# Optimization experiments

Measured on AMD Instinct MI355X. Metric: run time of the kernel, lower is better.

The kernel has to match this reference:

```python
import jax, jax.numpy as jnp
import numpy as np

# Config constants (MLAConfig)
B, S = 1, 2048                 # batch, context_len (prefill: seq == context_len)
H = 16                         # num_heads
DN, DR, DV = 128, 64, 128      # qk_nope_head_dim, qk_rope_head_dim, v_head_dim
QL, C = 1536, 512              # q_lora_rank, kv_lora_rank
BLK = 128                      # fp8 dequant block size
MAX_CACHE = 4096
SOFTMAX_SCALE = 1.0 / np.sqrt(DN + DR)  # 1/sqrt(192)
NEG_INF = -10000.0


def gen_rope(n_total, head_size):
    # theta_j = 10000^{-2j/d}; idx_theta[i, 0, :] = [i*theta, i*theta] (repeated halves)
    theta = 1.0 / (10000.0 ** (jnp.arange(0, head_size, 2, dtype=jnp.float32) / head_size))
    idx = jnp.outer(jnp.arange(n_total, dtype=jnp.float32), theta)  # (N, d/2)
    return jnp.tile(idx[:, None, :], (1, 1, 2))                     # (N, 1, d)


def fp8_dequant(x, s, block=BLK):
    # Block-wise dequant: x (M,N) * per-(block x block) scale s (M/b, N/b).
    M, N = x.shape
    m, n = M // block, N // block  # shapes chosen divisible by block -> no padding
    return (x.reshape(m, block, n, block) * s[:, None, :, None]).reshape(M, N)


def apply_rope(x, cos, sin):
    # x: (B*S, heads, d). Interleaved RoPE: de-interleave pairs into halves,
    # then x*cos + rotate_half(x)*sin with cos/sin (B*S, 1, d).
    bs, h, d = x.shape
    x = x.reshape(bs, h, d // 2, 2).transpose(0, 1, 3, 2).reshape(bs, h, d)
    rot = jnp.concatenate([-x[..., d // 2:], x[..., :d // 2]], axis=-1)
    return x * cos + rot * sin


def setup_inputs() -> dict:
    key = jax.random.key(0)
    ks = jax.random.split(key, 9)
    WUQ = jax.random.normal(ks[0], (H * (DN + DR), QL), dtype=jnp.float32)
    WUKV = jax.random.normal(ks[1], (H * (DN + DV), C), dtype=jnp.float32)
    # positive, small block scales so attention logits stay well-conditioned
    WUQ_scale = 0.05 * jax.random.uniform(ks[2], (H * (DN + DR) // BLK, QL // BLK), dtype=jnp.float32)
    WUKV_scale = 0.05 * jax.random.uniform(ks[3], (H * (DN + DV) // BLK, C // BLK), dtype=jnp.float32)
    Q = jax.random.normal(ks[4], (B, S, QL), dtype=jnp.float32)
    KV = jax.random.normal(ks[5], (B, S, C), dtype=jnp.float32)
    PE = jax.random.normal(ks[6], (B, S, DR), dtype=jnp.float32)
    kv_cache = jax.random.normal(ks[7], (B, MAX_CACHE, C), dtype=jnp.float32)
    pe_cache = jax.random.normal(ks[8], (B, MAX_CACHE, DR), dtype=jnp.float32)
    idx_theta = gen_rope(B * S, DR)
    mask = jnp.triu(jnp.full((S, S), NEG_INF, dtype=jnp.float32), k=1)
    return {"WUQ": WUQ, "WUQ_scale": WUQ_scale, "WUKV": WUKV, "WUKV_scale": WUKV_scale,
            "Q": Q, "KV": KV, "PE": PE, "kv_cache": kv_cache, "pe_cache": pe_cache,
            "idx_theta": idx_theta, "mask": mask}


def reference(WUQ, WUQ_scale, WUKV, WUKV_scale, Q, KV, PE, kv_cache, pe_cache, idx_theta, mask):
    bsz, seqlen, _ = Q.shape
    # fp8 block-wise dequant of the low-rank up-projection weights
    WUQd = fp8_dequant(WUQ, WUQ_scale)
    WUKVd = fp8_dequant(WUKV, WUKV_scale)
    # Q up-projection from q_lora latent: (B*S, QL) @ (QL, H*(DN+DR))
    q = (Q.reshape(-1, QL) @ WUQd.T).reshape(bsz, seqlen, H, DN + DR)
    q_nope, q_pe = q[..., :DN], q[..., DN:]
    cos, sin = jnp.cos(idx_theta), jnp.sin(idx_theta)  # (B*S, 1, DR)
    q_pe = apply_rope(q_pe.reshape(bsz * seqlen, H, DR), cos, sin).reshape(bsz, seqlen, H, DR)
    k_pe = apply_rope(PE.reshape(bsz * seqlen, 1, DR), cos, sin).reshape(bsz, seqlen, DR)
    # absorbed low-rank K matrix: q_nope projected into the kv latent space
    W3 = WUKVd.reshape(H, DN + DV, C)
    q_lat = jnp.einsum('bshd,hdc->bshc', q_nope, W3[:, :DN])
    # continuous-cache prefill: write fresh latents into the cache, attend over them
    kv = kv_cache.at[:, :seqlen].set(KV)[:, :seqlen]   # (B, S, C)
    pe = pe_cache.at[:, :seqlen].set(k_pe)[:, :seqlen]  # (B, S, DR)
    scores = (jnp.einsum('bshc,btc->bsht', q_lat, kv)
              + jnp.einsum('bshr,btr->bsht', q_pe, pe)) * SOFTMAX_SCALE
    scores = scores + mask[None, :, None, :]
    attn = jax.nn.softmax(scores, axis=-1)
    x = jnp.einsum('bsht,btc->bshc', attn, kv)
    out = jnp.einsum('bshc,hdc->bshd', x, W3[:, DN:])  # V up-projection (absorbed)
    return out  # (B, S, H, DV)
```

## Files before the change

### kernel.cpp

```cpp
#include <hip/hip_runtime.h>

typedef __bf16 bf16_t;
typedef __attribute__((ext_vector_type(4))) __bf16 bf16x4;
typedef __attribute__((ext_vector_type(8))) __bf16 bf16x8;
typedef __attribute__((ext_vector_type(4))) float f32x4;

#define SOFTMAX_SCALE 0.07216878364870322f
#define NEG_MASK (-10000.0f)

__device__ __forceinline__ void async16(const bf16_t* g, bf16_t* l) {
  __builtin_amdgcn_global_load_lds(
      (const __attribute__((address_space(1))) unsigned int*)g,
      (__attribute__((address_space(3))) unsigned int*)l, 16, 0, 0);
}


__global__ void k_dequant(const float* __restrict__ W, const float* __restrict__ S,
                          bf16_t* __restrict__ out, int cols, int scols) {
  int i = (blockIdx.x * 256 + threadIdx.x) * 4;
  int r = i / cols, c = i % cols;
  float s = S[(r >> 7) * scols + (c >> 7)];
  float4 w = *(const float4*)(W + i);
  out[i + 0] = (bf16_t)(w.x * s);
  out[i + 1] = (bf16_t)(w.y * s);
  out[i + 2] = (bf16_t)(w.z * s);
  out[i + 3] = (bf16_t)(w.w * s);
}

__global__ void k_f32_to_bf16(const float* __restrict__ in, bf16_t* __restrict__ out) {
  int i = (blockIdx.x * 256 + threadIdx.x) * 4;
  float4 v = *(const float4*)(in + i);
  out[i + 0] = (bf16_t)(v.x * SOFTMAX_SCALE);
  out[i + 1] = (bf16_t)(v.y * SOFTMAX_SCALE);
  out[i + 2] = (bf16_t)(v.z * SOFTMAX_SCALE);
  out[i + 3] = (bf16_t)(v.w * SOFTMAX_SCALE);
}

__global__ void k_wv1t(const bf16_t* __restrict__ Wd, bf16_t* __restrict__ Wt) {
  int i = blockIdx.x * 256 + threadIdx.x;
  int c = i & 511, d = (i >> 9) & 127, h = i >> 16;
  Wt[(h << 16) + (c << 7) + d] = Wd[((h << 8) + d) * 512 + c];
}

__global__ void k_k4(const float* __restrict__ KV, bf16_t* __restrict__ K4) {
  int i = blockIdx.x * 256 + threadIdx.x;
  int c2 = i & 15, t = i >> 4;
  int tt = t >> 6, k = t & 63;
  const float* src = KV + (size_t)t * 512 + c2 * 32;
  bf16_t* dst = K4 + (size_t)tt * 36864 + c2 * 2048 + k * 8;
#pragma unroll
  for (int sub = 0; sub < 4; ++sub) {
    float4 u = *(const float4*)(src + sub * 8);
    float4 v = *(const float4*)(src + sub * 8 + 4);
    bf16x8 o;
    o[0] = (bf16_t)u.x; o[1] = (bf16_t)u.y; o[2] = (bf16_t)u.z; o[3] = (bf16_t)u.w;
    o[4] = (bf16_t)v.x; o[5] = (bf16_t)v.y; o[6] = (bf16_t)v.z; o[7] = (bf16_t)v.w;
    *(bf16x8*)(dst + sub * 512) = o;
  }
}

__global__ void k_v4(const float* __restrict__ KV, bf16_t* __restrict__ V4) {
  int i = blockIdx.x * 256 + threadIdx.x;
  int c = i & 511, a = i >> 9;
  int t0 = a * 8, tt = t0 >> 6;
  int key0 = t0 & 63, kk2 = key0 >> 5, sub = (key0 >> 3) & 3;
  bf16x8 o;
#pragma unroll
  for (int j = 0; j < 8; ++j)
    o[j] = (bf16_t)KV[(size_t)(t0 + j) * 512 + c];
  *(bf16x8*)(V4 + (size_t)tt * 32768 + kk2 * 16384 + sub * 4096 + c * 8) = o;
}

__global__ void k_pe_rope(const float* __restrict__ PE, const float* __restrict__ idxt,
                          bf16_t* __restrict__ K4) {
  int i = blockIdx.x * 256 + threadIdx.x;
  int t = i >> 5, j = i & 31;
  float a = idxt[t * 64 + j];
  float c1 = cosf(a), s1 = sinf(a);
  float e = PE[t * 64 + 2 * j], o = PE[t * 64 + 2 * j + 1];
  int tt = t >> 6, k = t & 63;
  bf16_t* base = K4 + (size_t)tt * 36864 + (j >> 3) * 512 + k * 8 + (j & 7);
  base[16 * 2048] = (bf16_t)(e * c1 - o * s1);
  base[17 * 2048] = (bf16_t)(o * c1 + e * s1);
}

__global__ void k_q_rope(const bf16_t* __restrict__ q, const float* __restrict__ idxt,
                         bf16_t* __restrict__ qfull) {
  int i = blockIdx.x * 256 + threadIdx.x;
  int j = i & 31, h = (i >> 5) & 15, t = i >> 9;
  float a = idxt[t * 64 + j];
  float c1 = cosf(a), s1 = sinf(a);
  const bf16_t* src = q + t * 3072 + h * 192 + 128;
  float e = (float)src[2 * j], o = (float)src[2 * j + 1];
  bf16_t* dst = qfull + (size_t)h * 2048 * 576 + t * 576 + 512;
  dst[j]      = (bf16_t)(e * c1 - o * s1);
  dst[32 + j] = (bf16_t)(o * c1 + e * s1);
}

__global__ __launch_bounds__(256) void k_gemm2(const bf16_t* __restrict__ A,
                                               const bf16_t* __restrict__ B,
                                               bf16_t* __restrict__ C) {
  __shared__ __attribute__((aligned(16))) bf16_t At[2][8192];
  __shared__ __attribute__((aligned(16))) bf16_t Bt[2][8192];
  const int tid = threadIdx.x;
  const int lane = tid & 63;
  const int wv = tid >> 6;
  const int fr = lane & 15, fq = lane >> 4;
  const int wm = (wv & 1) * 64, wn = (wv >> 1) * 64;
  const int m0 = blockIdx.x * 128, n0 = blockIdx.y * 128;

#define STAGE2(bufp, ks)                                                    \
  do {                                                                      \
    _Pragma("unroll") for (int i_ = 0; i_ < 4; ++i_) {                      \
      int ch_ = tid + i_ * 256;                                             \
      int ar_ = ch_ >> 3;                                                   \
      int c8_ = (ch_ & 7) ^ (ar_ & 7);       \
      async16(A + (size_t)(m0 + ar_) * 1536 + (ks) * 64 + c8_ * 8,          \
              At[bufp] + ch_ * 8);                                          \
      async16(B + (size_t)(n0 + ar_) * 1536 + (ks) * 64 + c8_ * 8,          \
              Bt[bufp] + ch_ * 8);                                          \
    }                                                                       \
  } while (0)

  f32x4 acc[4][4] = {};
  STAGE2(0, 0);
  for (int ks = 0; ks < 24; ++ks) {
    int buf = ks & 1;
    __syncthreads();
    if (ks + 1 < 24) STAGE2(buf ^ 1, ks + 1);
#pragma unroll
    for (int kkl = 0; kkl < 2; ++kkl) {
      bf16x8 af[4], bfr[4];
#pragma unroll
      for (int m = 0; m < 4; ++m) {
        int row = wm + m * 16 + fr;
        af[m] = *(const bf16x8*)(At[buf] + (row * 8 + (((kkl * 4 + fq) ^ (row & 7)))) * 8);
      }
#pragma unroll
      for (int n = 0; n < 4; ++n) {
        int row = wn + n * 16 + fr;
        bfr[n] = *(const bf16x8*)(Bt[buf] + (row * 8 + (((kkl * 4 + fq) ^ (row & 7)))) * 8);
      }
#pragma unroll
      for (int m = 0; m < 4; ++m)
#pragma unroll
        for (int n = 0; n < 4; ++n)
          acc[m][n] = __builtin_amdgcn_mfma_f32_16x16x32_bf16(af[m], bfr[n], acc[m][n], 0, 0, 0);
    }
  }
#undef STAGE2
#pragma unroll
  for (int m = 0; m < 4; ++m) {
    int row = m0 + wm + m * 16 + fq * 4;
#pragma unroll
    for (int n = 0; n < 4; ++n) {
      int col = n0 + wn + n * 16 + fr;
#pragma unroll
      for (int i = 0; i < 4; ++i)
        C[(size_t)(row + i) * 3072 + col] = (bf16_t)acc[m][n][i];
    }
  }
}

template <int OUT_F32>
__global__ __launch_bounds__(256) void k_gemm(
    const bf16_t* __restrict__ A, int lda, long saz,
    const bf16_t* __restrict__ B, int ldb, long sbz,
    void* __restrict__ Cv, int ldc, long scz, int K) {
  __shared__ __attribute__((aligned(16))) bf16_t At[128 * 64];
  __shared__ __attribute__((aligned(16))) bf16_t Bt[128 * 64];
  const int tid = threadIdx.x;
  const int lane = tid & 63;
  const int wv = tid >> 6;
  const int fr = lane & 15, fq = lane >> 4;
  const int wm = (wv & 1) * 64, wn = (wv >> 1) * 64;
  const int m0 = blockIdx.x * 128, n0 = blockIdx.y * 128;
  const bf16_t* Ab = A + (long)blockIdx.z * saz;
  const bf16_t* Bb = B + (long)blockIdx.z * sbz;

  f32x4 acc[4][4] = {};
  bf16x8 va[4], vb[4];
#pragma unroll
  for (int j = 0; j < 4; ++j) {
    int ch = tid + j * 256, ar = ch >> 3, ac = (ch & 7) * 8;
    va[j] = *(const bf16x8*)(Ab + (size_t)(m0 + ar) * lda + ac);
    vb[j] = *(const bf16x8*)(Bb + (size_t)(n0 + ar) * ldb + ac);
  }

  for (int k0 = 0; k0 < K; k0 += 64) {
    __syncthreads();
#pragma unroll
    for (int j = 0; j < 4; ++j) {
      int ch = tid + j * 256, ar = ch >> 3, c8 = ch & 7;
      *(bf16x8*)(At + ar * 64 + ((c8 ^ (ar & 7)) * 8)) = va[j];
      *(bf16x8*)(Bt + ar * 64 + ((c8 ^ (ar & 7)) * 8)) = vb[j];
    }
    __syncthreads();
    if (k0 + 64 < K) {
#pragma unroll
      for (int j = 0; j < 4; ++j) {
        int ch = tid + j * 256, ar = ch >> 3, ac = (ch & 7) * 8;
        va[j] = *(const bf16x8*)(Ab + (size_t)(m0 + ar) * lda + k0 + 64 + ac);
        vb[j] = *(const bf16x8*)(Bb + (size_t)(n0 + ar) * ldb + k0 + 64 + ac);
      }
    }
#pragma unroll
    for (int kk = 0; kk < 2; ++kk) {
      bf16x8 af[4], bfr[4];
#pragma unroll
      for (int m = 0; m < 4; ++m)
        af[m] = *(const bf16x8*)(At + (wm + m * 16 + fr) * 64 + (((kk * 4 + fq) ^ (fr & 7)) * 8));
#pragma unroll
      for (int n = 0; n < 4; ++n)
        bfr[n] = *(const bf16x8*)(Bt + (wn + n * 16 + fr) * 64 + (((kk * 4 + fq) ^ (fr & 7)) * 8));
#pragma unroll
      for (int m = 0; m < 4; ++m)
#pragma unroll
        for (int n = 0; n < 4; ++n)
          acc[m][n] = __builtin_amdgcn_mfma_f32_16x16x32_bf16(af[m], bfr[n], acc[m][n], 0, 0, 0);
    }
  }
#pragma unroll
  for (int m = 0; m < 4; ++m) {
    int row = m0 + wm + m * 16 + fq * 4;
#pragma unroll
    for (int n = 0; n < 4; ++n) {
      int col = n0 + wn + n * 16 + fr;
#pragma unroll
      for (int i = 0; i < 4; ++i) {
        if (OUT_F32)
          ((float*)Cv)[(long)blockIdx.z * scz + (size_t)(row + i) * ldc + col] = acc[m][n][i];
        else
          ((bf16_t*)Cv)[(long)blockIdx.z * scz + (size_t)(row + i) * ldc + col] = (bf16_t)acc[m][n][i];
      }
    }
  }
}

__global__ __attribute__((amdgpu_flat_work_group_size(512, 512),
                          amdgpu_waves_per_eu(2, 2)))
void k_attn(const bf16_t* __restrict__ qfull,
            const bf16_t* __restrict__ K4,
            const bf16_t* __restrict__ V4,
            bf16_t* __restrict__ X) {
  __shared__ __attribute__((aligned(16))) bf16_t Kt[18 * 2048];
  __shared__ __attribute__((aligned(16))) bf16_t Vt[2 * 16384];
  __shared__ __attribute__((aligned(16))) bf16_t P[64 * 64];
  __shared__ __attribute__((aligned(16))) bf16_t Qpe[8 * 512];
  __shared__ float lred[4][64];

  const int tid = threadIdx.x;
  const int lane = tid & 63;
  const int w = tid >> 6;
  const int fr = lane & 15, fq = lane >> 4;
  const int h = blockIdx.x & 15;
  const int qt = 31 - (blockIdx.x >> 4);
  const int nt = qt + 1;
  const int rg = w >> 2;
  const int kq = w & 3;

  const bf16_t* qh = qfull + (size_t)h * 2048 * 576;
  bf16_t* Xh = X + (size_t)h * 2048 * 512;

  {
    int row = tid >> 3, sub = tid & 7;
    bf16x8 v = *(const bf16x8*)(qh + (size_t)(qt * 64 + row) * 576 + 512 + sub * 8);
    *(bf16x8*)(Qpe + sub * 512 + row * 8) = v;
  }

  bf16x8 qa[2][16];
  {
    const bf16_t* qb = qh + (size_t)(qt * 64 + rg * 32) * 576;
#pragma unroll
    for (int mf = 0; mf < 2; ++mf)
#pragma unroll
      for (int kk = 0; kk < 16; ++kk)
        qa[mf][kk] = *(const bf16x8*)(qb + (mf * 16 + fr) * 576 + kk * 32 + fq * 8);
  }

#pragma unroll
  for (int i = 0; i < 9; ++i) {
    int ck = w + 8 * i;
    async16(K4 + ck * 512 + lane * 8, Kt + ck * 512 + lane * 8);
  }

  f32x4 acc[2][8] = {};
  float lreg[2] = {0.f, 0.f};

  for (int t = 0; t < nt; ++t) {
    __syncthreads();

    {
      const bf16_t* vsrc = V4 + (size_t)t * 32768;
#pragma unroll
      for (int i = 0; i < 8; ++i) {
        int cv = w + 8 * i;
        async16(vsrc + cv * 512 + lane * 8, Vt + cv * 512 + lane * 8);
      }
    }

    f32x4 s[2] = {};
    __builtin_amdgcn_s_setprio(1);
#pragma unroll
    for (int kk = 0; kk < 16; ++kk) {
      bf16x8 kf = *(const bf16x8*)(Kt + kk * 2048 + fq * 512 + (kq * 16 + fr) * 8);
      s[0] = __builtin_amdgcn_mfma_f32_16x16x32_bf16(kf, qa[0][kk], s[0], 0, 0, 0);
      s[1] = __builtin_amdgcn_mfma_f32_16x16x32_bf16(kf, qa[1][kk], s[1], 0, 0, 0);
    }
#pragma unroll
    for (int kk = 16; kk < 18; ++kk) {
      bf16x8 kf = *(const bf16x8*)(Kt + kk * 2048 + fq * 512 + (kq * 16 + fr) * 8);
      bf16x8 q0 = *(const bf16x8*)(Qpe + ((kk - 16) * 4 + fq) * 512 + (rg * 32 + fr) * 8);
      bf16x8 q1 = *(const bf16x8*)(Qpe + ((kk - 16) * 4 + fq) * 512 + (rg * 32 + 16 + fr) * 8);
      s[0] = __builtin_amdgcn_mfma_f32_16x16x32_bf16(kf, q0, s[0], 0, 0, 0);
      s[1] = __builtin_amdgcn_mfma_f32_16x16x32_bf16(kf, q1, s[1], 0, 0, 0);
    }
    __builtin_amdgcn_s_setprio(0);

    bool diag = (t == qt);
#pragma unroll
    for (int mf = 0; mf < 2; ++mf) {
      int qrow = rg * 32 + mf * 16 + fr;
      if (diag) {
#pragma unroll
        for (int i = 0; i < 4; ++i) {
          int kcol = kq * 16 + fq * 4 + i;
          if (kcol > qrow) s[mf][i] += NEG_MASK;
        }
      }
      float p0 = __expf(s[mf][0]);
      float p1 = __expf(s[mf][1]);
      float p2 = __expf(s[mf][2]);
      float p3 = __expf(s[mf][3]);
      bf16x4 pk;
      pk[0] = (bf16_t)p0; pk[1] = (bf16_t)p1; pk[2] = (bf16_t)p2; pk[3] = (bf16_t)p3;
      int chunk = (kq * 2 + (fq >> 1)) ^ (qrow & 7);
      *(bf16x4*)(P + qrow * 64 + chunk * 8 + (fq & 1) * 4) = pk;
      lreg[mf] += (p0 + p1) + (p2 + p3);
    }
    __syncthreads();

    if (t + 1 < nt) {
      const bf16_t* ksrc = K4 + (size_t)(t + 1) * 36864;
#pragma unroll
      for (int i = 0; i < 9; ++i) {
        int ck = w + 8 * i;
        async16(ksrc + ck * 512 + lane * 8, Kt + ck * 512 + lane * 8);
      }
    }

    __builtin_amdgcn_s_setprio(1);
#pragma unroll
    for (int kk2 = 0; kk2 < 2; ++kk2) {
      bf16x8 pa[2];
#pragma unroll
      for (int mf = 0; mf < 2; ++mf) {
        int qrow = rg * 32 + mf * 16 + fr;
        pa[mf] = *(const bf16x8*)(P + qrow * 64 + (((kk2 * 4 + fq) ^ (qrow & 7)) * 8));
      }
#pragma unroll
      for (int nf = 0; nf < 8; ++nf) {
        bf16x8 vb = *(const bf16x8*)(Vt + kk2 * 16384 + fq * 4096 + (kq * 128 + nf * 16 + fr) * 8);
        acc[0][nf] = __builtin_amdgcn_mfma_f32_16x16x32_bf16(pa[0], vb, acc[0][nf], 0, 0, 0);
        acc[1][nf] = __builtin_amdgcn_mfma_f32_16x16x32_bf16(pa[1], vb, acc[1][nf], 0, 0, 0);
      }
    }
    __builtin_amdgcn_s_setprio(0);
  }

#pragma unroll
  for (int mf = 0; mf < 2; ++mf) {
    float lw = lreg[mf];
    lw += __shfl_xor(lw, 16);
    lw += __shfl_xor(lw, 32);
    if (fq == 0) lred[kq][rg * 32 + mf * 16 + fr] = lw;
  }
  __syncthreads();

  {
    bf16_t* XT = Kt;
#pragma unroll
    for (int mf = 0; mf < 2; ++mf)
#pragma unroll
      for (int i = 0; i < 4; ++i) {
        int row = rg * 32 + mf * 16 + fq * 4 + i;
        float invl = 1.0f / ((lred[0][row] + lred[1][row]) + (lred[2][row] + lred[3][row]));
#pragma unroll
        for (int nf = 0; nf < 8; ++nf)
          XT[row * 512 + kq * 128 + nf * 16 + fr] = (bf16_t)(acc[mf][nf][i] * invl);
      }
  }
  __syncthreads();
#pragma unroll
  for (int it = 0; it < 8; ++it) {
    int id = tid + it * 512;
    int row = id >> 6, j = id & 63;
    *(bf16x8*)(Xh + (size_t)(qt * 64 + row) * 512 + j * 8) = *(const bf16x8*)(Kt + row * 512 + j * 8);
  }
}


extern "C" void kernel_launch(void* const* d_in, const int* in_sizes, int n_in,
                              void* d_out, int out_size, void* d_ws, size_t ws_size,
                              hipStream_t stream) {
  (void)in_sizes; (void)n_in; (void)out_size; (void)ws_size;
  const float* WUQ   = (const float*)d_in[0];
  const float* WUQs  = (const float*)d_in[1];
  const float* WUKV  = (const float*)d_in[2];
  const float* WUKVs = (const float*)d_in[3];
  const float* Q     = (const float*)d_in[4];
  const float* KV    = (const float*)d_in[5];
  const float* PE    = (const float*)d_in[6];
  const float* idxt  = (const float*)d_in[9];
  float* out = (float*)d_out;

  char* ws = (char*)d_ws;
  size_t off = 0;
  auto alloc = [&](size_t n) -> char* {
    char* p = ws + off;
    off += (n + 255) & ~(size_t)255;
    return p;
  };
  bf16_t* WUQd  = (bf16_t*)alloc((size_t)3072 * 1536 * 2);
  bf16_t* Qb    = (bf16_t*)alloc((size_t)2048 * 1536 * 2);
  bf16_t* WUKVd = (bf16_t*)alloc((size_t)4096 * 512 * 2);
  bf16_t* Wv1t  = (bf16_t*)alloc((size_t)16 * 512 * 128 * 2);
  bf16_t* qbuf  = (bf16_t*)alloc((size_t)2048 * 3072 * 2);
  bf16_t* K4    = (bf16_t*)alloc((size_t)32 * 36864 * 2);
  bf16_t* V4    = (bf16_t*)alloc((size_t)32 * 32768 * 2);
  bf16_t* qfull = (bf16_t*)alloc((size_t)16 * 2048 * 576 * 2);
  bf16_t* Xb    = (bf16_t*)alloc((size_t)16 * 2048 * 512 * 2);

  k_dequant<<<4608, 256, 0, stream>>>(WUQ, WUQs, WUQd, 1536, 12);
  k_dequant<<<2048, 256, 0, stream>>>(WUKV, WUKVs, WUKVd, 512, 4);
  k_f32_to_bf16<<<3072, 256, 0, stream>>>(Q, Qb);
  k_wv1t<<<4096, 256, 0, stream>>>(WUKVd, Wv1t);
  k_k4<<<128, 256, 0, stream>>>(KV, K4);
  k_v4<<<512, 256, 0, stream>>>(KV, V4);
  k_pe_rope<<<256, 256, 0, stream>>>(PE, idxt, K4);
  k_gemm2<<<dim3(16, 24), 256, 0, stream>>>(Qb, WUQd, qbuf);
  k_q_rope<<<4096, 256, 0, stream>>>(qbuf, idxt, qfull);
  k_gemm<0><<<dim3(16, 4, 16), 256, 0, stream>>>(qbuf, 3072, 192, Wv1t, 128, (long)512 * 128,
                                                 qfull, 576, (long)2048 * 576, 128);
  k_attn<<<dim3(512), dim3(512), 0, stream>>>(qfull, K4, V4, Xb);
  k_gemm<1><<<dim3(16, 1, 16), 256, 0, stream>>>(Xb, 512, (long)2048 * 512,
                                                 WUKVd + 128 * 512, 512, (long)256 * 512,
                                                 out, 2048, 128, 512);
}
```

Measured before the change: 208.7 us.

## Unify GEMMs on async double-buffered kernel, tile Wv1 transpose, split QK accumulators

Generalizes the async global-to-LDS double-buffered GEMM into a templated batched kernel and uses it for all three projection GEMMs, replacing the register-staged single-buffer GEMM. The per-element weight transpose kernel becomes an LDS-tiled transpose with vectorized 16-byte loads and stores. In attention, the QK score accumulation is split into two independent accumulator chains that are summed afterwards, shortening the MFMA dependency chain. The changes cost more LDS per GEMM block, a few extra registers in attention, and a different floating-point summation order for the scores.

Measured after the change: 203.7 us. -2.4%, faster.

```diff
diff --git a/kernel.cpp b/kernel.cpp
--- a/kernel.cpp
+++ b/kernel.cpp
@@ -37,9 +37,26 @@
 }
 
 __global__ void k_wv1t(const bf16_t* __restrict__ Wd, bf16_t* __restrict__ Wt) {
-  int i = blockIdx.x * 256 + threadIdx.x;
-  int c = i & 511, d = (i >> 9) & 127, h = i >> 16;
-  Wt[(h << 16) + (c << 7) + d] = Wd[((h << 8) + d) * 512 + c];
+  __shared__ bf16_t Lt[64][72];
+  int h = blockIdx.x >> 4;
+  int d0 = ((blockIdx.x >> 3) & 1) * 64;
+  int c0 = (blockIdx.x & 7) * 64;
+  int t = threadIdx.x;
+#pragma unroll
+  for (int j = 0; j < 2; ++j) {
+    int ch = t * 2 + j, r = ch >> 3, c8 = ch & 7;
+    bf16x8 v = *(const bf16x8*)(Wd + (size_t)(h * 256 + d0 + r) * 512 + c0 + c8 * 8);
+    *(bf16x8*)&Lt[r][c8 * 8] = v;
+  }
+  __syncthreads();
+#pragma unroll
+  for (int j = 0; j < 2; ++j) {
+    int ch = t * 2 + j, cc = ch >> 3, dd8 = ch & 7;
+    bf16x8 o;
+#pragma unroll
+    for (int e = 0; e < 8; ++e) o[e] = Lt[dd8 * 8 + e][cc];
+    *(bf16x8*)(Wt + (size_t)h * 65536 + (c0 + cc) * 128 + d0 + dd8 * 8) = o;
+  }
 }
 
 __global__ void k_k4(const float* __restrict__ KV, bf16_t* __restrict__ K4) {
@@ -97,9 +114,11 @@
   dst[32 + j] = (bf16_t)(o * c1 + e * s1);
 }
 
-__global__ __launch_bounds__(256) void k_gemm2(const bf16_t* __restrict__ A,
-                                               const bf16_t* __restrict__ B,
-                                               bf16_t* __restrict__ C) {
+template <int OUT_F32>
+__global__ __launch_bounds__(256) void k_gemm3(
+    const bf16_t* __restrict__ A, int lda, long saz,
+    const bf16_t* __restrict__ B, int ldb, long sbz,
+    void* __restrict__ Cv, int ldc, long scz, int K) {
   __shared__ __attribute__((aligned(16))) bf16_t At[2][8192];
   __shared__ __attribute__((aligned(16))) bf16_t Bt[2][8192];
   const int tid = threadIdx.x;
@@ -108,26 +127,29 @@
   const int fr = lane & 15, fq = lane >> 4;
   const int wm = (wv & 1) * 64, wn = (wv >> 1) * 64;
   const int m0 = blockIdx.x * 128, n0 = blockIdx.y * 128;
-
-#define STAGE2(bufp, ks)                                                    \
+  const bf16_t* Ab = A + (long)blockIdx.z * saz;
+  const bf16_t* Bb = B + (long)blockIdx.z * sbz;
+
+#define STAGE3(bufp, ks)                                                    \
   do {                                                                      \
     _Pragma("unroll") for (int i_ = 0; i_ < 4; ++i_) {                      \
       int ch_ = tid + i_ * 256;                                             \
       int ar_ = ch_ >> 3;                                                   \
-      int c8_ = (ch_ & 7) ^ (ar_ & 7);       \
-      async16(A + (size_t)(m0 + ar_) * 1536 + (ks) * 64 + c8_ * 8,          \
+      int c8_ = (ch_ & 7) ^ (ar_ & 7);                                      \
+      async16(Ab + (size_t)(m0 + ar_) * lda + (ks) * 64 + c8_ * 8,          \
               At[bufp] + ch_ * 8);                                          \
-      async16(B + (size_t)(n0 + ar_) * 1536 + (ks) * 64 + c8_ * 8,          \
+      async16(Bb + (size_t)(n0 + ar_) * ldb + (ks) * 64 + c8_ * 8,          \
               Bt[bufp] + ch_ * 8);                                          \
     }                                                                       \
   } while (0)
 
   f32x4 acc[4][4] = {};
-  STAGE2(0, 0);
-  for (int ks = 0; ks < 24; ++ks) {
+  const int nks = K >> 6;
+  STAGE3(0, 0);
+  for (int ks = 0; ks < nks; ++ks) {
     int buf = ks & 1;
     __syncthreads();
-    if (ks + 1 < 24) STAGE2(buf ^ 1, ks + 1);
+    if (ks + 1 < nks) STAGE3(buf ^ 1, ks + 1);
 #pragma unroll
     for (int kkl = 0; kkl < 2; ++kkl) {
       bf16x8 af[4], bfr[4];
@@ -148,78 +170,7 @@
           acc[m][n] = __builtin_amdgcn_mfma_f32_16x16x32_bf16(af[m], bfr[n], acc[m][n], 0, 0, 0);
     }
   }
-#undef STAGE2
-#pragma unroll
-  for (int m = 0; m < 4; ++m) {
-    int row = m0 + wm + m * 16 + fq * 4;
-#pragma unroll
-    for (int n = 0; n < 4; ++n) {
-      int col = n0 + wn + n * 16 + fr;
-#pragma unroll
-      for (int i = 0; i < 4; ++i)
-        C[(size_t)(row + i) * 3072 + col] = (bf16_t)acc[m][n][i];
-    }
-  }
-}
-
-template <int OUT_F32>
-__global__ __launch_bounds__(256) void k_gemm(
-    const bf16_t* __restrict__ A, int lda, long saz,
-    const bf16_t* __restrict__ B, int ldb, long sbz,
-    void* __restrict__ Cv, int ldc, long scz, int K) {
-  __shared__ __attribute__((aligned(16))) bf16_t At[128 * 64];
-  __shared__ __attribute__((aligned(16))) bf16_t Bt[128 * 64];
-  const int tid = threadIdx.x;
-  const int lane = tid & 63;
-  const int wv = tid >> 6;
-  const int fr = lane & 15, fq = lane >> 4;
-  const int wm = (wv & 1) * 64, wn = (wv >> 1) * 64;
-  const int m0 = blockIdx.x * 128, n0 = blockIdx.y * 128;
-  const bf16_t* Ab = A + (long)blockIdx.z * saz;
-  const bf16_t* Bb = B + (long)blockIdx.z * sbz;
-
-  f32x4 acc[4][4] = {};
-  bf16x8 va[4], vb[4];
-#pragma unroll
-  for (int j = 0; j < 4; ++j) {
-    int ch = tid + j * 256, ar = ch >> 3, ac = (ch & 7) * 8;
-    va[j] = *(const bf16x8*)(Ab + (size_t)(m0 + ar) * lda + ac);
-    vb[j] = *(const bf16x8*)(Bb + (size_t)(n0 + ar) * ldb + ac);
-  }
-
-  for (int k0 = 0; k0 < K; k0 += 64) {
-    __syncthreads();
-#pragma unroll
-    for (int j = 0; j < 4; ++j) {
-      int ch = tid + j * 256, ar = ch >> 3, c8 = ch & 7;
-      *(bf16x8*)(At + ar * 64 + ((c8 ^ (ar & 7)) * 8)) = va[j];
-      *(bf16x8*)(Bt + ar * 64 + ((c8 ^ (ar & 7)) * 8)) = vb[j];
-    }
-    __syncthreads();
-    if (k0 + 64 < K) {
-#pragma unroll
-      for (int j = 0; j < 4; ++j) {
-        int ch = tid + j * 256, ar = ch >> 3, ac = (ch & 7) * 8;
-        va[j] = *(const bf16x8*)(Ab + (size_t)(m0 + ar) * lda + k0 + 64 + ac);
-        vb[j] = *(const bf16x8*)(Bb + (size_t)(n0 + ar) * ldb + k0 + 64 + ac);
-      }
-    }
-#pragma unroll
-    for (int kk = 0; kk < 2; ++kk) {
-      bf16x8 af[4], bfr[4];
-#pragma unroll
-      for (int m = 0; m < 4; ++m)
-        af[m] = *(const bf16x8*)(At + (wm + m * 16 + fr) * 64 + (((kk * 4 + fq) ^ (fr & 7)) * 8));
-#pragma unroll
-      for (int n = 0; n < 4; ++n)
-        bfr[n] = *(const bf16x8*)(Bt + (wn + n * 16 + fr) * 64 + (((kk * 4 + fq) ^ (fr & 7)) * 8));
-#pragma unroll
-      for (int m = 0; m < 4; ++m)
-#pragma unroll
-        for (int n = 0; n < 4; ++n)
-          acc[m][n] = __builtin_amdgcn_mfma_f32_16x16x32_bf16(af[m], bfr[n], acc[m][n], 0, 0, 0);
-    }
-  }
+#undef STAGE3
 #pragma unroll
   for (int m = 0; m < 4; ++m) {
     int row = m0 + wm + m * 16 + fq * 4;
@@ -299,23 +250,35 @@
       }
     }
 
-    f32x4 s[2] = {};
+    f32x4 sA[2] = {}, sB[2] = {};
     __builtin_amdgcn_s_setprio(1);
 #pragma unroll
-    for (int kk = 0; kk < 16; ++kk) {
-      bf16x8 kf = *(const bf16x8*)(Kt + kk * 2048 + fq * 512 + (kq * 16 + fr) * 8);
-      s[0] = __builtin_amdgcn_mfma_f32_16x16x32_bf16(kf, qa[0][kk], s[0], 0, 0, 0);
-      s[1] = __builtin_amdgcn_mfma_f32_16x16x32_bf16(kf, qa[1][kk], s[1], 0, 0, 0);
-    }
-#pragma unroll
-    for (int kk = 16; kk < 18; ++kk) {
-      bf16x8 kf = *(const bf16x8*)(Kt + kk * 2048 + fq * 512 + (kq * 16 + fr) * 8);
-      bf16x8 q0 = *(const bf16x8*)(Qpe + ((kk - 16) * 4 + fq) * 512 + (rg * 32 + fr) * 8);
-      bf16x8 q1 = *(const bf16x8*)(Qpe + ((kk - 16) * 4 + fq) * 512 + (rg * 32 + 16 + fr) * 8);
-      s[0] = __builtin_amdgcn_mfma_f32_16x16x32_bf16(kf, q0, s[0], 0, 0, 0);
-      s[1] = __builtin_amdgcn_mfma_f32_16x16x32_bf16(kf, q1, s[1], 0, 0, 0);
+    for (int kk = 0; kk < 16; kk += 2) {
+      bf16x8 kf0 = *(const bf16x8*)(Kt + kk * 2048 + fq * 512 + (kq * 16 + fr) * 8);
+      bf16x8 kf1 = *(const bf16x8*)(Kt + (kk + 1) * 2048 + fq * 512 + (kq * 16 + fr) * 8);
+      sA[0] = __builtin_amdgcn_mfma_f32_16x16x32_bf16(kf0, qa[0][kk], sA[0], 0, 0, 0);
+      sA[1] = __builtin_amdgcn_mfma_f32_16x16x32_bf16(kf0, qa[1][kk], sA[1], 0, 0, 0);
+      sB[0] = __builtin_amdgcn_mfma_f32_16x16x32_bf16(kf1, qa[0][kk + 1], sB[0], 0, 0, 0);
+      sB[1] = __builtin_amdgcn_mfma_f32_16x16x32_bf16(kf1, qa[1][kk + 1], sB[1], 0, 0, 0);
+    }
+    {
+      bf16x8 kf0 = *(const bf16x8*)(Kt + 16 * 2048 + fq * 512 + (kq * 16 + fr) * 8);
+      bf16x8 kf1 = *(const bf16x8*)(Kt + 17 * 2048 + fq * 512 + (kq * 16 + fr) * 8);
+      bf16x8 q00 = *(const bf16x8*)(Qpe + fq * 512 + (rg * 32 + fr) * 8);
+      bf16x8 q01 = *(const bf16x8*)(Qpe + fq * 512 + (rg * 32 + 16 + fr) * 8);
+      bf16x8 q10 = *(const bf16x8*)(Qpe + (4 + fq) * 512 + (rg * 32 + fr) * 8);
+      bf16x8 q11 = *(const bf16x8*)(Qpe + (4 + fq) * 512 + (rg * 32 + 16 + fr) * 8);
+      sA[0] = __builtin_amdgcn_mfma_f32_16x16x32_bf16(kf0, q00, sA[0], 0, 0, 0);
+      sA[1] = __builtin_amdgcn_mfma_f32_16x16x32_bf16(kf0, q01, sA[1], 0, 0, 0);
+      sB[0] = __builtin_amdgcn_mfma_f32_16x16x32_bf16(kf1, q10, sB[0], 0, 0, 0);
+      sB[1] = __builtin_amdgcn_mfma_f32_16x16x32_bf16(kf1, q11, sB[1], 0, 0, 0);
     }
     __builtin_amdgcn_s_setprio(0);
+    f32x4 s[2];
+#pragma unroll
+    for (int mf = 0; mf < 2; ++mf)
+#pragma unroll
+      for (int i = 0; i < 4; ++i) s[mf][i] = sA[mf][i] + sB[mf][i];
 
     bool diag = (t == qt);
 #pragma unroll
@@ -434,16 +397,17 @@
   k_dequant<<<4608, 256, 0, stream>>>(WUQ, WUQs, WUQd, 1536, 12);
   k_dequant<<<2048, 256, 0, stream>>>(WUKV, WUKVs, WUKVd, 512, 4);
   k_f32_to_bf16<<<3072, 256, 0, stream>>>(Q, Qb);
-  k_wv1t<<<4096, 256, 0, stream>>>(WUKVd, Wv1t);
+  k_wv1t<<<256, 256, 0, stream>>>(WUKVd, Wv1t);
   k_k4<<<128, 256, 0, stream>>>(KV, K4);
   k_v4<<<512, 256, 0, stream>>>(KV, V4);
   k_pe_rope<<<256, 256, 0, stream>>>(PE, idxt, K4);
-  k_gemm2<<<dim3(16, 24), 256, 0, stream>>>(Qb, WUQd, qbuf);
+  k_gemm3<0><<<dim3(16, 24, 1), 256, 0, stream>>>(Qb, 1536, 0, WUQd, 1536, 0,
+                                                  qbuf, 3072, 0, 1536);
   k_q_rope<<<4096, 256, 0, stream>>>(qbuf, idxt, qfull);
-  k_gemm<0><<<dim3(16, 4, 16), 256, 0, stream>>>(qbuf, 3072, 192, Wv1t, 128, (long)512 * 128,
-                                                 qfull, 576, (long)2048 * 576, 128);
+  k_gemm3<0><<<dim3(16, 4, 16), 256, 0, stream>>>(qbuf, 3072, 192, Wv1t, 128, (long)512 * 128,
+                                                  qfull, 576, (long)2048 * 576, 128);
   k_attn<<<dim3(512), dim3(512), 0, stream>>>(qfull, K4, V4, Xb);
-  k_gemm<1><<<dim3(16, 1, 16), 256, 0, stream>>>(Xb, 512, (long)2048 * 512,
-                                                 WUKVd + 128 * 512, 512, (long)256 * 512,
-                                                 out, 2048, 128, 512);
-}
+  k_gemm3<1><<<dim3(16, 1, 16), 256, 0, stream>>>(Xb, 512, (long)2048 * 512,
+                                                  WUKVd + 128 * 512, 512, (long)256 * 512,
+                                                  out, 2048, 128, 512);
+}
```
